# Performance work log

Hardware: AMD Instinct MI355X
Metric: run time of the kernel (lower is better)

Reference implementation:

```python
import jax, jax.numpy as jnp
import numpy as np

B, T, C = 16, 2048, 128
HEAD_SIZE = 128

def setup_inputs() -> dict:
    key = jax.random.key(0)
    k1, k2, k3, k4 = jax.random.split(key, 4)
    x = jax.random.normal(k1, (B, T, C), dtype=jnp.float32)
    # nn.Linear(N_EMBED, head_size, bias=False) weight shape: [head_size, N_EMBED]
    scale = (1.0 / np.sqrt(C)).astype(np.float32)
    Wq = jax.random.normal(k2, (HEAD_SIZE, C), dtype=jnp.float32) * scale
    Wk = jax.random.normal(k3, (HEAD_SIZE, C), dtype=jnp.float32) * scale
    Wv = jax.random.normal(k4, (HEAD_SIZE, C), dtype=jnp.float32) * scale
    return {"x": x, "Wq": Wq, "Wk": Wk, "Wv": Wv}

def reference(x, Wq, Wk, Wv):
    Bd, Td, Cd = x.shape
    q = jnp.einsum('btc,hc->bth', x, Wq)  # [B,T,H]
    k = jnp.einsum('btc,hc->bth', x, Wk)
    v = jnp.einsum('btc,hc->bth', x, Wv)
    # NOTE: original scales by C**-0.5 (embedding dim), not head_size**-0.5
    scores = jnp.einsum('bth,bsh->bts', q, k) * (Cd ** -0.5)  # [B,T,T]
    causal = jnp.tril(jnp.ones((Td, Td), dtype=bool))
    scores = jnp.where(causal, scores, -jnp.inf)
    attn = jax.nn.softmax(scores, axis=-1)
    out = jnp.einsum('bts,bsh->bth', attn, v)  # [B,T,H]
    return out
```

## Files before the change

kernel.cpp:

```cpp
#include <hip/hip_runtime.h>
#include <hip/hip_bf16.h>

#define BB 16
#define TT 2048
#define CC 128
#define HH 128
#define NQT128 16

typedef __bf16 bf16x8 __attribute__((ext_vector_type(8)));
typedef float  f32x4  __attribute__((ext_vector_type(4)));

#define BTH       ((size_t)BB * TT * HH)
#define WBF_OFF   (3 * BTH)
#define PARTIAL_OFF_BYTES (3 * BTH * 2 + 3 * 128 * 128 * 2)
#define SLOT_FLOATS (128 * 128 + 128)

static __device__ __forceinline__ bf16x8 load_cvt8(const float* __restrict__ p) {
    float4 a = *(const float4*)p;
    float4 b = *(const float4*)(p + 4);
    bf16x8 r;
    r[0] = (__bf16)a.x; r[1] = (__bf16)a.y; r[2] = (__bf16)a.z; r[3] = (__bf16)a.w;
    r[4] = (__bf16)b.x; r[5] = (__bf16)b.y; r[6] = (__bf16)b.z; r[7] = (__bf16)b.w;
    return r;
}

static __device__ __forceinline__ void load_lds16(const void* g, void* l) {
    __builtin_amdgcn_global_load_lds(
        (const __attribute__((address_space(1))) unsigned int*)g,
        (__attribute__((address_space(3))) unsigned int*)l, 16, 0, 0);
}

__global__ __launch_bounds__(256) void wcvt_kernel(
    const float* __restrict__ Wq, const float* __restrict__ Wk,
    const float* __restrict__ Wv, __bf16* __restrict__ wbf)
{
    int idx = blockIdx.x * 256 + threadIdx.x;
    int m = idx >> 14;
    int e = idx & 16383;
    const float* src = (m == 0) ? Wq : (m == 1) ? Wk : Wv;
    float sc = (m == 0) ? (0.08838834764831845f * 1.4426950408889634f) : 1.0f;
    wbf[idx] = (__bf16)(src[e] * sc);
}

#define TR_QK 132
#define TR_V  68

__global__ __launch_bounds__(256) void proj_kernel(
    const float* __restrict__ x, __bf16* __restrict__ ws)
{
    __shared__ __bf16 tr[128 * TR_V];

    const int lane = threadIdx.x & 63;
    const int wave = threadIdx.x >> 6;
    const int quad = lane >> 4;
    const int l16  = lane & 15;
    const int m0 = blockIdx.x * 64;
    const int b  = m0 / TT;
    const int t0 = m0 % TT;

    const __bf16* Wbf = ws + WBF_OFF;
    __bf16* Qs = ws;
    __bf16* Ks = ws + BTH;
    __bf16* Vs = ws + 2 * BTH;

    bf16x8 xf[4];
    #pragma unroll
    for (int ks = 0; ks < 4; ++ks)
        xf[ks] = load_cvt8(x + (size_t)(m0 + wave * 16 + l16) * CC + ks * 32 + quad * 8);

    #pragma unroll
    for (int which = 0; which < 2; ++which) {
        const __bf16* Wb = Wbf + (size_t)which * (128 * 128);
        __bf16* dst = which ? Ks : Qs;
        #pragma unroll
        for (int nt = 0; nt < 8; ++nt) {
            f32x4 acc = {0.f, 0.f, 0.f, 0.f};
            #pragma unroll
            for (int ks = 0; ks < 4; ++ks) {
                bf16x8 wf = *(const bf16x8*)(Wb + (size_t)(nt * 16 + l16) * CC + ks * 32 + quad * 8);
                acc = __builtin_amdgcn_mfma_f32_16x16x32_bf16(xf[ks], wf, acc, 0, 0, 0);
            }
            #pragma unroll
            for (int r = 0; r < 4; ++r)
                tr[(wave * 16 + quad * 4 + r) * TR_QK + nt * 16 + l16] = (__bf16)acc[r];
        }
        asm volatile("s_waitcnt lgkmcnt(0)" ::: "memory");
        #pragma unroll
        for (int ks = 0; ks < 4; ++ks) {
            const __bf16* p = &tr[(wave * 16 + l16) * TR_QK + ks * 32 + quad * 8];
            uint2 lo = *(const uint2*)p;
            uint2 hi = *(const uint2*)(p + 4);
            uint4 v; v.x = lo.x; v.y = lo.y; v.z = hi.x; v.w = hi.y;
            __bf16* o = dst + (((size_t)(b * 128 + t0 / 16 + wave) * 4 + ks) << 9) + lane * 8;
            *(uint4*)o = v;
        }
        asm volatile("s_waitcnt lgkmcnt(0)" ::: "memory");
    }

    __syncthreads();
    const __bf16* Wv = Wbf + 2 * (128 * 128);
    #pragma unroll
    for (int msub = 0; msub < 8; ++msub) {
        f32x4 acc = {0.f, 0.f, 0.f, 0.f};
        #pragma unroll
        for (int ks = 0; ks < 4; ++ks) {
            bf16x8 wf = *(const bf16x8*)(Wv + (size_t)(msub * 16 + l16) * CC + ks * 32 + quad * 8);
            acc = __builtin_amdgcn_mfma_f32_16x16x32_bf16(wf, xf[ks], acc, 0, 0, 0);
        }
        #pragma unroll
        for (int r = 0; r < 4; ++r)
            tr[(msub * 16 + quad * 4 + r) * TR_V + wave * 16 + l16] = (__bf16)acc[r];
    }
    __syncthreads();
    #pragma unroll
    for (int i = 0; i < 4; ++i) {
        int t32 = i >> 1;
        int h16 = wave * 2 + (i & 1);
        const __bf16* p = &tr[(h16 * 16 + l16) * TR_V + t32 * 32 + quad * 8];
        uint2 lo = *(const uint2*)p;
        uint2 hi = *(const uint2*)(p + 4);
        uint4 v; v.x = lo.x; v.y = lo.y; v.z = hi.x; v.w = hi.y;
        __bf16* o = Vs + (((size_t)(b * 64 + t0 / 32 + t32) * 8 + h16) << 9) + lane * 8;
        *(uint4*)o = v;
    }
}

#define S_LDS 76
#define EXP_BIAS 16.0f

__global__ __launch_bounds__(256) void attn_kernel(
    const __bf16* __restrict__ ws, float* __restrict__ po,
    float* __restrict__ outp, int G, int SPB, int direct)
{
    __shared__ __bf16 ldsK[8192];
    __shared__ __bf16 ldsV[8192];
    __shared__ __bf16 lds_p[4 * 32 * S_LDS];

    const int lane = threadIdx.x & 63;
    const int wave = threadIdx.x >> 6;
    const int quad = lane >> 4;
    const int l16  = lane & 15;
    const int lane8 = lane * 8;

    const int lin = blockIdx.x;
    const int b  = (lin & 7) * 2 + ((lin >> 3) & 1);
    const int s  = SPB - 1 - (lin >> 4);

    int acc = 0, qt = 0, seg = 0;
    for (int q = 0; q < NQT128; ++q) {
        int c = (2 * (q + 1) + G - 1) / G;
        if (s < acc + c) { qt = q; seg = s - acc; break; }
        acc += c;
    }
    const int kt0 = seg * G;
    int kt1 = 2 * (qt + 1);
    if (kt0 + G < kt1) kt1 = kt0 + G;

    const int qw = qt * 128 + wave * 32;
    int kt1w = (qw + 32 + 63) >> 6;
    if (kt1w > kt1) kt1w = kt1;

    const __bf16* Qs = ws;
    const __bf16* Ks = ws + BTH;
    const __bf16* Vs = ws + 2 * BTH;

    bf16x8 qf[2][4];
    #pragma unroll
    for (int m = 0; m < 2; ++m)
        #pragma unroll
        for (int ks = 0; ks < 4; ++ks)
            qf[m][ks] = *(const bf16x8*)(Qs + (((size_t)(b * 128 + qt * 8 + wave * 2 + m) * 4 + ks) << 9) + lane8);

    float l_r[2][4];
    f32x4 o[2][8];
    #pragma unroll
    for (int m = 0; m < 2; ++m) {
        #pragma unroll
        for (int r = 0; r < 4; ++r) l_r[m][r] = 0.f;
        #pragma unroll
        for (int h8 = 0; h8 < 8; ++h8) o[m][h8] = (f32x4){0.f, 0.f, 0.f, 0.f};
    }

    __bf16* myP = lds_p + wave * 32 * S_LDS;

    for (int kt = kt0; kt < kt1; ++kt) {
        const char* kbase = (const char*)(Ks + (((size_t)(b * 128 + kt * 4) * 4) << 9));
        const char* vbase = (const char*)(Vs + (((size_t)(b * 64 + kt * 2) * 8) << 9));
        #pragma unroll
        for (int i = 0; i < 8; ++i) {
            const int c = wave * 8 + i;
            const char* g = (c < 16) ? (kbase + c * 1024) : (vbase + (c - 16) * 1024);
            char* l = (c < 16) ? ((char*)ldsK + c * 1024) : ((char*)ldsV + (c - 16) * 1024);
            load_lds16(g + (size_t)lane * 16, l);
        }
        asm volatile("s_waitcnt vmcnt(0)" ::: "memory");
        __syncthreads();

        if (kt < kt1w) {
            const int k0 = kt * 64;

            f32x4 s2[2][4];
            #pragma unroll
            for (int nsub = 0; nsub < 4; ++nsub) {
                bf16x8 kfr[4];
                #pragma unroll
                for (int ks = 0; ks < 4; ++ks)
                    kfr[ks] = *(const bf16x8*)((const char*)ldsK + ((nsub * 4 + ks) << 10) + lane * 16);
                #pragma unroll
                for (int m = 0; m < 2; ++m) {
                    f32x4 a2 = {0.f, 0.f, 0.f, 0.f};
                    #pragma unroll
                    for (int ks = 0; ks < 4; ++ks)
                        a2 = __builtin_amdgcn_mfma_f32_16x16x32_bf16(qf[m][ks], kfr[ks], a2, 0, 0, 0);
                    s2[m][nsub] = a2;
                }
            }

            #pragma unroll
            for (int m = 0; m < 2; ++m) {
                const int qr0m = qw + m * 16;
                if (k0 + 63 > qr0m) {
                    #pragma unroll
                    for (int nsub = 0; nsub < 4; ++nsub) {
                        int key = k0 + nsub * 16 + l16;
                        #pragma unroll
                        for (int r = 0; r < 4; ++r) {
                            int rowq = qr0m + quad * 4 + r;
                            if (key > rowq) s2[m][nsub][r] = -3e38f;
                        }
                    }
                }
                #pragma unroll
                for (int nsub = 0; nsub < 4; ++nsub) {
                    #pragma unroll
                    for (int r = 0; r < 4; ++r) {
                        float p = __builtin_amdgcn_exp2f(s2[m][nsub][r] - EXP_BIAS);
                        l_r[m][r] += p;
                        myP[(m * 16 + quad * 4 + r) * S_LDS + nsub * 16 + l16] = (__bf16)p;
                    }
                }
            }
            asm volatile("s_waitcnt lgkmcnt(0)" ::: "memory");

            bf16x8 pf[2][2];
            #pragma unroll
            for (int m = 0; m < 2; ++m)
                #pragma unroll
                for (int ks2 = 0; ks2 < 2; ++ks2) {
                    union { bf16x8 v; uint2 h[2]; } u;
                    const char* base = (const char*)myP + (size_t)(m * 16 + l16) * (S_LDS * 2) + ks2 * 64 + quad * 16;
                    u.h[0] = *(const uint2*)base;
                    u.h[1] = *(const uint2*)(base + 8);
                    pf[m][ks2] = u.v;
                }

            #pragma unroll
            for (int h8 = 0; h8 < 8; ++h8) {
                bf16x8 v0 = *(const bf16x8*)((const char*)ldsV + ((0 * 8 + h8) << 10) + lane * 16);
                bf16x8 v1 = *(const bf16x8*)((const char*)ldsV + ((1 * 8 + h8) << 10) + lane * 16);
                #pragma unroll
                for (int m = 0; m < 2; ++m) {
                    o[m][h8] = __builtin_amdgcn_mfma_f32_16x16x32_bf16(pf[m][0], v0, o[m][h8], 0, 0, 0);
                    o[m][h8] = __builtin_amdgcn_mfma_f32_16x16x32_bf16(pf[m][1], v1, o[m][h8], 0, 0, 0);
                }
            }
        }
        __syncthreads();
    }

    #pragma unroll
    for (int m = 0; m < 2; ++m)
        #pragma unroll
        for (int r = 0; r < 4; ++r)
            #pragma unroll
            for (int j = 1; j <= 8; j <<= 1)
                l_r[m][r] += __shfl_xor(l_r[m][r], j, 64);

    if (direct) {
        #pragma unroll
        for (int m = 0; m < 2; ++m) {
            float inv[4];
            #pragma unroll
            for (int r = 0; r < 4; ++r) inv[r] = 1.0f / l_r[m][r];
            #pragma unroll
            for (int h8 = 0; h8 < 8; ++h8)
                #pragma unroll
                for (int r = 0; r < 4; ++r)
                    outp[(size_t)(b * TT + qw + m * 16 + quad * 4 + r) * HH + h8 * 16 + l16] = o[m][h8][r] * inv[r];
        }
    } else {
        float* slot = po + (size_t)(b * SPB + s) * SLOT_FLOATS;
        #pragma unroll
        for (int m = 0; m < 2; ++m) {
            #pragma unroll
            for (int h8 = 0; h8 < 8; ++h8)
                #pragma unroll
                for (int r = 0; r < 4; ++r)
                    slot[(size_t)(wave * 32 + m * 16 + quad * 4 + r) * HH + h8 * 16 + l16] = o[m][h8][r];
            if (l16 == 0) {
                #pragma unroll
                for (int r = 0; r < 4; ++r)
                    slot[128 * 128 + wave * 32 + m * 16 + quad * 4 + r] = l_r[m][r];
            }
        }
    }
}

__global__ __launch_bounds__(256) void reduce_kernel(
    const float* __restrict__ po, float* __restrict__ outp, int G, int SPB)
{
    __shared__ float lsum[32];
    const int qt  = blockIdx.x >> 2;
    const int qtr = blockIdx.x & 3;
    const int b   = blockIdx.y;
    const int tid = threadIdx.x;

    int acc = 0;
    for (int qq = 0; qq < qt; ++qq) acc += (2 * (qq + 1) + G - 1) / G;
    const int segs = (2 * (qt + 1) + G - 1) / G;
    const float* base = po + (size_t)(b * SPB + acc) * SLOT_FLOATS;
    const int r0 = qtr * 32;

    if (tid < 32) {
        float v = 0.f;
        for (int sg = 0; sg < segs; ++sg)
            v += base[(size_t)sg * SLOT_FLOATS + 128 * 128 + r0 + tid];
        lsum[tid] = v;
    }
    __syncthreads();

    const int f4c  = tid & 31;
    const int rowg = tid >> 5;
    float4 a[4];
    #pragma unroll
    for (int p = 0; p < 4; ++p) a[p] = (float4){0.f, 0.f, 0.f, 0.f};

    for (int sg = 0; sg < segs; ++sg) {
        const float* sb = base + (size_t)sg * SLOT_FLOATS;
        #pragma unroll
        for (int p = 0; p < 4; ++p) {
            int row = r0 + p * 8 + rowg;
            float4 v = *(const float4*)(sb + (size_t)row * 128 + f4c * 4);
            a[p].x += v.x; a[p].y += v.y; a[p].z += v.z; a[p].w += v.w;
        }
    }

    #pragma unroll
    for (int p = 0; p < 4; ++p) {
        int row = r0 + p * 8 + rowg;
        float inv = 1.0f / lsum[p * 8 + rowg];
        float4 o4 = {a[p].x * inv, a[p].y * inv, a[p].z * inv, a[p].w * inv};
        *(float4*)(outp + (size_t)(b * TT + qt * 128 + row) * HH + f4c * 4) = o4;
    }
}

extern "C" void kernel_launch(void* const* d_in, const int* in_sizes, int n_in,
                              void* d_out, int out_size, void* d_ws, size_t ws_size,
                              hipStream_t stream)
{
    const float* x  = (const float*)d_in[0];
    const float* Wq = (const float*)d_in[1];
    const float* Wk = (const float*)d_in[2];
    const float* Wv = (const float*)d_in[3];
    __bf16* ws = (__bf16*)d_ws;
    float* out = (float*)d_out;
    float* po  = (float*)((char*)d_ws + PARTIAL_OFF_BYTES);

    int G = 0, SPB = 0, direct = 1;
    const int cand[3] = {6, 8, 16};
    for (int ci = 0; ci < 3; ++ci) {
        int g = cand[ci], spb = 0;
        for (int q = 0; q < NQT128; ++q) spb += (2 * (q + 1) + g - 1) / g;
        size_t need = PARTIAL_OFF_BYTES + (size_t)spb * BB * SLOT_FLOATS * 4;
        if (need <= ws_size) { G = g; SPB = spb; direct = 0; break; }
    }
    if (direct) { G = 2 * NQT128; SPB = NQT128; }

    wcvt_kernel<<<192, 256, 0, stream>>>(Wq, Wk, Wv, ws + WBF_OFF);
    proj_kernel<<<512, 256, 0, stream>>>(x, ws);
    attn_kernel<<<SPB * 16, 256, 0, stream>>>(ws, po, out, G, SPB, direct);
    if (!direct) {
        dim3 rgrid(NQT128 * 4, BB);
        reduce_kernel<<<rgrid, 256, 0, stream>>>(po, out, G, SPB);
    }
}
```

Before: 150.0 us.

## Prefetch K/V tiles, store partials in bf16, pre-swizzle weights, stage x via LDS

The attention loop now prefetches the next K tile after the score MFMAs and the next V tile after the PV step, with split barriers, so global-to-LDS loads overlap compute. Split-K partial outputs are stored in bf16 instead of fp32 to cut workspace traffic. Query tiles with only one segment write the final output directly, and the reduce kernel returns early for them. Weights are converted into the MFMA fragment layout so proj loads are contiguous, and x is staged through LDS with coalesced loads. The bf16 partials lose some precision, and the single-buffered LDS prefetch depends on the barriers being placed correctly.

```diff
diff --git a/kernel.cpp b/kernel.cpp
--- a/kernel.cpp
+++ b/kernel.cpp
@@ -13,9 +13,10 @@
 #define BTH       ((size_t)BB * TT * HH)
 #define WBF_OFF   (3 * BTH)
 #define PARTIAL_OFF_BYTES (3 * BTH * 2 + 3 * 128 * 128 * 2)
-#define SLOT_FLOATS (128 * 128 + 128)
-
-static __device__ __forceinline__ bf16x8 load_cvt8(const float* __restrict__ p) {
+#define SLOT_BYTES 33280
+#define SLOT_L_OFF 32768
+
+static __device__ __forceinline__ bf16x8 load_cvt8(const float* p) {
     float4 a = *(const float4*)p;
     float4 b = *(const float4*)(p + 4);
     bf16x8 r;
@@ -30,16 +31,28 @@
         (__attribute__((address_space(3))) unsigned int*)l, 16, 0, 0);
 }
 
+#define BAR_VM()   asm volatile("s_waitcnt vmcnt(0)\n\ts_barrier" ::: "memory")
+#define BAR_LGKM() asm volatile("s_waitcnt lgkmcnt(0)\n\ts_barrier" ::: "memory")
+
 __global__ __launch_bounds__(256) void wcvt_kernel(
     const float* __restrict__ Wq, const float* __restrict__ Wk,
     const float* __restrict__ Wv, __bf16* __restrict__ wbf)
 {
     int idx = blockIdx.x * 256 + threadIdx.x;
-    int m = idx >> 14;
-    int e = idx & 16383;
-    const float* src = (m == 0) ? Wq : (m == 1) ? Wk : Wv;
-    float sc = (m == 0) ? (0.08838834764831845f * 1.4426950408889634f) : 1.0f;
-    wbf[idx] = (__bf16)(src[e] * sc);
+    int which = idx >> 11;
+    int rem = idx & 2047;
+    int blk = rem >> 8;
+    int r2  = rem & 255;
+    int ks   = r2 >> 6;
+    int lane = r2 & 63;
+    int quad = lane >> 4, l16 = lane & 15;
+    const float* src = (which == 0) ? Wq : (which == 1) ? Wk : Wv;
+    float sc = (which == 0) ? (0.08838834764831845f * 1.4426950408889634f) : 1.0f;
+    const float* p = src + (size_t)(blk * 16 + l16) * CC + ks * 32 + quad * 8;
+    bf16x8 v;
+    #pragma unroll
+    for (int j = 0; j < 8; ++j) v[j] = (__bf16)(p[j] * sc);
+    *(bf16x8*)(wbf + (size_t)which * 16384 + (((size_t)(blk * 4 + ks)) << 9) + lane * 8) = v;
 }
 
 #define TR_QK 132
@@ -48,12 +61,14 @@
 __global__ __launch_bounds__(256) void proj_kernel(
     const float* __restrict__ x, __bf16* __restrict__ ws)
 {
+    __shared__ float  xs[64 * 132];
     __shared__ __bf16 tr[128 * TR_V];
 
     const int lane = threadIdx.x & 63;
     const int wave = threadIdx.x >> 6;
     const int quad = lane >> 4;
     const int l16  = lane & 15;
+    const int tid  = threadIdx.x;
     const int m0 = blockIdx.x * 64;
     const int b  = m0 / TT;
     const int t0 = m0 % TT;
@@ -63,21 +78,31 @@
     __bf16* Ks = ws + BTH;
     __bf16* Vs = ws + 2 * BTH;
 
+    const float* xg = x + (size_t)m0 * CC;
+    #pragma unroll
+    for (int t = 0; t < 8; ++t) {
+        int f = t * 256 + tid;
+        int row = f >> 5, c4 = f & 31;
+        float4 v = *(const float4*)(xg + (size_t)f * 4);
+        *(float4*)(&xs[row * 132 + c4 * 4]) = v;
+    }
+    __syncthreads();
+
     bf16x8 xf[4];
     #pragma unroll
     for (int ks = 0; ks < 4; ++ks)
-        xf[ks] = load_cvt8(x + (size_t)(m0 + wave * 16 + l16) * CC + ks * 32 + quad * 8);
+        xf[ks] = load_cvt8(&xs[(wave * 16 + l16) * 132 + ks * 32 + quad * 8]);
 
     #pragma unroll
     for (int which = 0; which < 2; ++which) {
-        const __bf16* Wb = Wbf + (size_t)which * (128 * 128);
+        const __bf16* Wb = Wbf + (size_t)which * 16384;
         __bf16* dst = which ? Ks : Qs;
         #pragma unroll
         for (int nt = 0; nt < 8; ++nt) {
             f32x4 acc = {0.f, 0.f, 0.f, 0.f};
             #pragma unroll
             for (int ks = 0; ks < 4; ++ks) {
-                bf16x8 wf = *(const bf16x8*)(Wb + (size_t)(nt * 16 + l16) * CC + ks * 32 + quad * 8);
+                bf16x8 wf = *(const bf16x8*)(Wb + (((size_t)(nt * 4 + ks)) << 9) + lane * 8);
                 acc = __builtin_amdgcn_mfma_f32_16x16x32_bf16(xf[ks], wf, acc, 0, 0, 0);
             }
             #pragma unroll
@@ -98,13 +123,13 @@
     }
 
     __syncthreads();
-    const __bf16* Wv = Wbf + 2 * (128 * 128);
+    const __bf16* Wv = Wbf + 2 * 16384;
     #pragma unroll
     for (int msub = 0; msub < 8; ++msub) {
         f32x4 acc = {0.f, 0.f, 0.f, 0.f};
         #pragma unroll
         for (int ks = 0; ks < 4; ++ks) {
-            bf16x8 wf = *(const bf16x8*)(Wv + (size_t)(msub * 16 + l16) * CC + ks * 32 + quad * 8);
+            bf16x8 wf = *(const bf16x8*)(Wv + (((size_t)(msub * 4 + ks)) << 9) + lane * 8);
             acc = __builtin_amdgcn_mfma_f32_16x16x32_bf16(wf, xf[ks], acc, 0, 0, 0);
         }
         #pragma unroll
@@ -129,7 +154,7 @@
 #define EXP_BIAS 16.0f
 
 __global__ __launch_bounds__(256) void attn_kernel(
-    const __bf16* __restrict__ ws, float* __restrict__ po,
+    const __bf16* __restrict__ ws, char* __restrict__ po,
     float* __restrict__ outp, int G, int SPB, int direct)
 {
     __shared__ __bf16 ldsK[8192];
@@ -155,6 +180,8 @@
     const int kt0 = seg * G;
     int kt1 = 2 * (qt + 1);
     if (kt0 + G < kt1) kt1 = kt0 + G;
+    const int segs_qt = (2 * (qt + 1) + G - 1) / G;
+    const int dwrite = direct | (segs_qt == 1);
 
     const int qw = qt * 128 + wave * 32;
     int kt1w = (qw + 32 + 63) >> 6;
@@ -183,23 +210,33 @@
 
     __bf16* myP = lds_p + wave * 32 * S_LDS;
 
+    #define STAGE_K(KT)                                                             \
+        do {                                                                        \
+            const char* kb_ = (const char*)(Ks + (((size_t)(b * 128 + (KT) * 4) * 4) << 9)); \
+            _Pragma("unroll")                                                       \
+            for (int i_ = 0; i_ < 4; ++i_) {                                        \
+                int c_ = wave * 4 + i_;                                             \
+                load_lds16(kb_ + c_ * 1024 + (size_t)lane * 16, (char*)ldsK + c_ * 1024); \
+            }                                                                       \
+        } while (0)
+    #define STAGE_V(KT)                                                             \
+        do {                                                                        \
+            const char* vb_ = (const char*)(Vs + (((size_t)(b * 64 + (KT) * 2) * 8) << 9)); \
+            _Pragma("unroll")                                                       \
+            for (int i_ = 0; i_ < 4; ++i_) {                                        \
+                int c_ = wave * 4 + i_;                                             \
+                load_lds16(vb_ + c_ * 1024 + (size_t)lane * 16, (char*)ldsV + c_ * 1024); \
+            }                                                                       \
+        } while (0)
+
+    STAGE_K(kt0);
+    STAGE_V(kt0);
+
     for (int kt = kt0; kt < kt1; ++kt) {
-        const char* kbase = (const char*)(Ks + (((size_t)(b * 128 + kt * 4) * 4) << 9));
-        const char* vbase = (const char*)(Vs + (((size_t)(b * 64 + kt * 2) * 8) << 9));
-        #pragma unroll
-        for (int i = 0; i < 8; ++i) {
-            const int c = wave * 8 + i;
-            const char* g = (c < 16) ? (kbase + c * 1024) : (vbase + (c - 16) * 1024);
-            char* l = (c < 16) ? ((char*)ldsK + c * 1024) : ((char*)ldsV + (c - 16) * 1024);
-            load_lds16(g + (size_t)lane * 16, l);
-        }
-        asm volatile("s_waitcnt vmcnt(0)" ::: "memory");
-        __syncthreads();
-
+        BAR_VM();
+
+        f32x4 s2[2][4];
         if (kt < kt1w) {
-            const int k0 = kt * 64;
-
-            f32x4 s2[2][4];
             #pragma unroll
             for (int nsub = 0; nsub < 4; ++nsub) {
                 bf16x8 kfr[4];
@@ -215,7 +252,12 @@
                     s2[m][nsub] = a2;
                 }
             }
-
+        }
+        BAR_LGKM();
+        if (kt + 1 < kt1) STAGE_K(kt + 1);
+
+        if (kt < kt1w) {
+            const int k0 = kt * 64;
             #pragma unroll
             for (int m = 0; m < 2; ++m) {
                 const int qr0m = qw + m * 16;
@@ -265,7 +307,8 @@
                 }
             }
         }
-        __syncthreads();
+        BAR_LGKM();
+        if (kt + 1 < kt1) STAGE_V(kt + 1);
     }
 
     #pragma unroll
@@ -276,7 +319,7 @@
             for (int j = 1; j <= 8; j <<= 1)
                 l_r[m][r] += __shfl_xor(l_r[m][r], j, 64);
 
-    if (direct) {
+    if (dwrite) {
         #pragma unroll
         for (int m = 0; m < 2; ++m) {
             float inv[4];
@@ -289,25 +332,27 @@
                     outp[(size_t)(b * TT + qw + m * 16 + quad * 4 + r) * HH + h8 * 16 + l16] = o[m][h8][r] * inv[r];
         }
     } else {
-        float* slot = po + (size_t)(b * SPB + s) * SLOT_FLOATS;
+        char* slot = po + (size_t)(b * SPB + s) * SLOT_BYTES;
+        __bf16* slot_o = (__bf16*)slot;
+        float*  slot_l = (float*)(slot + SLOT_L_OFF);
         #pragma unroll
         for (int m = 0; m < 2; ++m) {
             #pragma unroll
             for (int h8 = 0; h8 < 8; ++h8)
                 #pragma unroll
                 for (int r = 0; r < 4; ++r)
-                    slot[(size_t)(wave * 32 + m * 16 + quad * 4 + r) * HH + h8 * 16 + l16] = o[m][h8][r];
+                    slot_o[(size_t)(wave * 32 + m * 16 + quad * 4 + r) * 128 + h8 * 16 + l16] = (__bf16)o[m][h8][r];
             if (l16 == 0) {
                 #pragma unroll
                 for (int r = 0; r < 4; ++r)
-                    slot[128 * 128 + wave * 32 + m * 16 + quad * 4 + r] = l_r[m][r];
+                    slot_l[wave * 32 + m * 16 + quad * 4 + r] = l_r[m][r];
             }
         }
     }
 }
 
 __global__ __launch_bounds__(256) void reduce_kernel(
-    const float* __restrict__ po, float* __restrict__ outp, int G, int SPB)
+    const char* __restrict__ po, float* __restrict__ outp, int G, int SPB)
 {
     __shared__ float lsum[32];
     const int qt  = blockIdx.x >> 2;
@@ -315,42 +360,51 @@
     const int b   = blockIdx.y;
     const int tid = threadIdx.x;
 
+    const int segs = (2 * (qt + 1) + G - 1) / G;
+    if (segs == 1) return;
+
     int acc = 0;
     for (int qq = 0; qq < qt; ++qq) acc += (2 * (qq + 1) + G - 1) / G;
-    const int segs = (2 * (qt + 1) + G - 1) / G;
-    const float* base = po + (size_t)(b * SPB + acc) * SLOT_FLOATS;
+    const char* base = po + (size_t)(b * SPB + acc) * SLOT_BYTES;
     const int r0 = qtr * 32;
 
     if (tid < 32) {
         float v = 0.f;
         for (int sg = 0; sg < segs; ++sg)
-            v += base[(size_t)sg * SLOT_FLOATS + 128 * 128 + r0 + tid];
+            v += ((const float*)(base + (size_t)sg * SLOT_BYTES + SLOT_L_OFF))[r0 + tid];
         lsum[tid] = v;
     }
     __syncthreads();
 
-    const int f4c  = tid & 31;
-    const int rowg = tid >> 5;
-    float4 a[4];
-    #pragma unroll
-    for (int p = 0; p < 4; ++p) a[p] = (float4){0.f, 0.f, 0.f, 0.f};
+    const int rsub = tid >> 4;
+    const int cg   = tid & 15;
+    float a[2][8];
+    #pragma unroll
+    for (int p = 0; p < 2; ++p)
+        #pragma unroll
+        for (int j = 0; j < 8; ++j) a[p][j] = 0.f;
 
     for (int sg = 0; sg < segs; ++sg) {
-        const float* sb = base + (size_t)sg * SLOT_FLOATS;
-        #pragma unroll
-        for (int p = 0; p < 4; ++p) {
-            int row = r0 + p * 8 + rowg;
-            float4 v = *(const float4*)(sb + (size_t)row * 128 + f4c * 4);
-            a[p].x += v.x; a[p].y += v.y; a[p].z += v.z; a[p].w += v.w;
-        }
-    }
-
-    #pragma unroll
-    for (int p = 0; p < 4; ++p) {
-        int row = r0 + p * 8 + rowg;
-        float inv = 1.0f / lsum[p * 8 + rowg];
-        float4 o4 = {a[p].x * inv, a[p].y * inv, a[p].z * inv, a[p].w * inv};
-        *(float4*)(outp + (size_t)(b * TT + qt * 128 + row) * HH + f4c * 4) = o4;
+        const char* sb = base + (size_t)sg * SLOT_BYTES;
+        #pragma unroll
+        for (int p = 0; p < 2; ++p) {
+            int row = r0 + rsub + p * 16;
+            union { uint4 u; __bf16 h[8]; } v;
+            v.u = *(const uint4*)(sb + ((size_t)row * 128 + cg * 8) * 2);
+            #pragma unroll
+            for (int j = 0; j < 8; ++j) a[p][j] += (float)v.h[j];
+        }
+    }
+
+    #pragma unroll
+    for (int p = 0; p < 2; ++p) {
+        int row = r0 + rsub + p * 16;
+        float inv = 1.0f / lsum[rsub + p * 16];
+        float* op = outp + (size_t)(b * TT + qt * 128 + row) * HH + cg * 8;
+        float4 o0 = {a[p][0] * inv, a[p][1] * inv, a[p][2] * inv, a[p][3] * inv};
+        float4 o1 = {a[p][4] * inv, a[p][5] * inv, a[p][6] * inv, a[p][7] * inv};
+        *(float4*)op = o0;
+        *(float4*)(op + 4) = o1;
     }
 }
 
@@ -364,19 +418,19 @@
     const float* Wv = (const float*)d_in[3];
     __bf16* ws = (__bf16*)d_ws;
     float* out = (float*)d_out;
-    float* po  = (float*)((char*)d_ws + PARTIAL_OFF_BYTES);
+    char* po   = (char*)d_ws + PARTIAL_OFF_BYTES;
 
     int G = 0, SPB = 0, direct = 1;
     const int cand[3] = {6, 8, 16};
     for (int ci = 0; ci < 3; ++ci) {
         int g = cand[ci], spb = 0;
         for (int q = 0; q < NQT128; ++q) spb += (2 * (q + 1) + g - 1) / g;
-        size_t need = PARTIAL_OFF_BYTES + (size_t)spb * BB * SLOT_FLOATS * 4;
+        size_t need = PARTIAL_OFF_BYTES + (size_t)spb * BB * SLOT_BYTES;
         if (need <= ws_size) { G = g; SPB = spb; direct = 0; break; }
     }
     if (direct) { G = 2 * NQT128; SPB = NQT128; }
 
-    wcvt_kernel<<<192, 256, 0, stream>>>(Wq, Wk, Wv, ws + WBF_OFF);
+    wcvt_kernel<<<24, 256, 0, stream>>>(Wq, Wk, Wv, ws + WBF_OFF);
     proj_kernel<<<512, 256, 0, stream>>>(x, ws);
     attn_kernel<<<SPB * 16, 256, 0, stream>>>(ws, po, out, G, SPB, direct);
     if (!direct) {
```

Measured after the change: 143.4 us. -4.4%, faster.
